# Kernel optimization log

Measured on AMD Instinct MI355X. Metric: run time of the kernel, lower is better.

The kernel has to match this reference:

```python
import jax, jax.numpy as jnp
import numpy as np


def setup_inputs() -> dict:
    key = jax.random.key(0)
    x = jax.random.normal(key, (32, 1, 1024, 1024), dtype=jnp.float32)
    return {"x": x}


def reference(x) -> jnp.ndarray:
    # Original torch loop computes a running max down the height dim (dim=2)
    # for channel 0 (C=1 here), overwriting each element with the prefix max.
    # This is exactly a cumulative-max (prefix-max scan) along axis=2.
    return jax.lax.associative_scan(jnp.maximum, x, axis=2)
```

## Files before the change

### kernel.cpp

```cpp
#include <hip/hip_runtime.h>


constexpr int B = 32;
constexpr int H = 1024;
constexpr int W = 1024;
constexpr int ROW4 = W / 4;
constexpr int SW4 = 8;
constexpr int NSTRIP = ROW4 / SW4;
constexpr int CH = 128;
constexpr int NCHUNK = H / CH;
constexpr int NT = 256;
constexpr int SEG = 32;
constexpr int RPS = CH / SEG;
constexpr int LPT = CH * SW4 / NT;

typedef float floatx4 __attribute__((ext_vector_type(4)));

__device__ __forceinline__ float4 max4(float4 a, float4 b) {
    return make_float4(fmaxf(a.x, b.x), fmaxf(a.y, b.y),
                       fmaxf(a.z, b.z), fmaxf(a.w, b.w));
}

__global__ __launch_bounds__(256) void cummax_onepass(const float* __restrict__ xf,
                                                      float* __restrict__ of) {
    __shared__ float4 buf[2][CH * SW4];
    __shared__ float4 smax[SEG][SW4];

    const int tid = threadIdx.x;
    const int b = blockIdx.x >> 5;
    const int strip = blockIdx.x & (NSTRIP - 1);
    const float4* x4 = (const float4*)xf;
    float* out_f = of;
    const size_t base4 = (size_t)b * (H * ROW4) + (size_t)strip * SW4;

    const int s = tid >> 3;
    const int wg = tid & 7;

    const float ninf = -__builtin_inff();
    float4 carry = make_float4(ninf, ninf, ninf, ninf);

    float4 ld[LPT];

#pragma unroll
    for (int i = 0; i < LPT; ++i) {
        const int e = i * NT + tid;
        const int hl = e >> 3, w = e & 7;
        ld[i] = x4[base4 + (size_t)hl * ROW4 + w];
    }
#pragma unroll
    for (int i = 0; i < LPT; ++i) buf[0][i * NT + tid] = ld[i];
    __syncthreads();

    for (int c = 0; c < NCHUNK; ++c) {
        const int cb = c & 1, nb = cb ^ 1;

        if (c + 1 < NCHUNK) {
#pragma unroll
            for (int i = 0; i < LPT; ++i) {
                const int e = i * NT + tid;
                const int hl = e >> 3, w = e & 7;
                ld[i] = x4[base4 + (size_t)((c + 1) * CH + hl) * ROW4 + w];
            }
        }

        float4 m = buf[cb][(s * RPS) * SW4 + wg];
#pragma unroll
        for (int r = 1; r < RPS; ++r) m = max4(m, buf[cb][(s * RPS + r) * SW4 + wg]);
        smax[s][wg] = m;
        __syncthreads();

        float4 pre = carry, tot = carry;
#pragma unroll
        for (int s2 = 0; s2 < SEG; ++s2) {
            const float4 v = smax[s2][wg];
            if (s2 < s) pre = max4(pre, v);
            tot = max4(tot, v);
        }
        carry = tot;

        float4 a = pre;
#pragma unroll
        for (int r = 0; r < RPS; ++r) {
            a = max4(a, buf[cb][(s * RPS + r) * SW4 + wg]);
            const size_t o = base4 + (size_t)(c * CH + s * RPS + r) * ROW4 + wg;
            floatx4 av = {a.x, a.y, a.z, a.w};
            __builtin_nontemporal_store(av, (floatx4*)out_f + o);
        }

        if (c + 1 < NCHUNK) {
#pragma unroll
            for (int i = 0; i < LPT; ++i) buf[nb][i * NT + tid] = ld[i];
        }
        __syncthreads();
    }
}

extern "C" void kernel_launch(void* const* d_in, const int* in_sizes, int n_in,
                              void* d_out, int out_size, void* d_ws, size_t ws_size,
                              hipStream_t stream) {
    const float* x = (const float*)d_in[0];
    float* out = (float*)d_out;
    cummax_onepass<<<B * NSTRIP, NT, 0, stream>>>(x, out);
}
```

Before: 257.2 us.

## Replace shared-memory chunk scan with register-resident wavefront shuffle scan

Each thread now keeps its 4 rows of the chunk in registers instead of staging the whole chunk through a double-buffered LDS tile. Segment maxima are scanned within each wavefront using shuffle-up steps, and only per-wave totals go through a small shared array. This cuts LDS traffic and removes one barrier per chunk. It also drops the nontemporal store hint, which may change cache behaviour on output writes.

```diff
diff --git a/kernel.cpp b/kernel.cpp
--- a/kernel.cpp
+++ b/kernel.cpp
@@ -9,89 +9,90 @@
 constexpr int NSTRIP = ROW4 / SW4;
 constexpr int CH = 128;
 constexpr int NCHUNK = H / CH;
-constexpr int NT = 256;
-constexpr int SEG = 32;
-constexpr int RPS = CH / SEG;
-constexpr int LPT = CH * SW4 / NT;
-
-typedef float floatx4 __attribute__((ext_vector_type(4)));
+constexpr int R = 4;
 
 __device__ __forceinline__ float4 max4(float4 a, float4 b) {
     return make_float4(fmaxf(a.x, b.x), fmaxf(a.y, b.y),
                        fmaxf(a.z, b.z), fmaxf(a.w, b.w));
 }
 
-__global__ __launch_bounds__(256) void cummax_onepass(const float* __restrict__ xf,
-                                                      float* __restrict__ of) {
-    __shared__ float4 buf[2][CH * SW4];
-    __shared__ float4 smax[SEG][SW4];
+__device__ __forceinline__ float4 shflup4(float4 v, int d) {
+    float4 r;
+    r.x = __shfl_up(v.x, d, 64);
+    r.y = __shfl_up(v.y, d, 64);
+    r.z = __shfl_up(v.z, d, 64);
+    r.w = __shfl_up(v.w, d, 64);
+    return r;
+}
+
+__global__ __launch_bounds__(256) void cummax_sp(const float* __restrict__ xf,
+                                                 float* __restrict__ of) {
+    __shared__ float4 wavetot[2][32];
 
     const int tid = threadIdx.x;
+    const int lane = tid & 63;
+    const int wid = tid >> 6;
+    const int w = tid & 7;
+    const int hsegG = tid >> 3;
+    const int hseg_l = (tid >> 3) & 7;
+
     const int b = blockIdx.x >> 5;
     const int strip = blockIdx.x & (NSTRIP - 1);
     const float4* x4 = (const float4*)xf;
-    float* out_f = of;
-    const size_t base4 = (size_t)b * (H * ROW4) + (size_t)strip * SW4;
-
-    const int s = tid >> 3;
-    const int wg = tid & 7;
+    float4* o4 = (float4*)of;
+    const size_t tbase = (size_t)b * (H * ROW4) + (size_t)strip * SW4 + w;
 
     const float ninf = -__builtin_inff();
-    float4 carry = make_float4(ninf, ninf, ninf, ninf);
+    const float4 ninf4 = make_float4(ninf, ninf, ninf, ninf);
+    float4 carry = ninf4;
 
-    float4 ld[LPT];
+    float4 cur[R], nxt[R];
 
 #pragma unroll
-    for (int i = 0; i < LPT; ++i) {
-        const int e = i * NT + tid;
-        const int hl = e >> 3, w = e & 7;
-        ld[i] = x4[base4 + (size_t)hl * ROW4 + w];
-    }
+    for (int r = 0; r < R; ++r)
+        cur[r] = x4[tbase + (size_t)(hsegG * R + r) * ROW4];
+
 #pragma unroll
-    for (int i = 0; i < LPT; ++i) buf[0][i * NT + tid] = ld[i];
-    __syncthreads();
-
     for (int c = 0; c < NCHUNK; ++c) {
-        const int cb = c & 1, nb = cb ^ 1;
-
         if (c + 1 < NCHUNK) {
 #pragma unroll
-            for (int i = 0; i < LPT; ++i) {
-                const int e = i * NT + tid;
-                const int hl = e >> 3, w = e & 7;
-                ld[i] = x4[base4 + (size_t)((c + 1) * CH + hl) * ROW4 + w];
-            }
+            for (int r = 0; r < R; ++r)
+                nxt[r] = x4[tbase + (size_t)((c + 1) * CH + hsegG * R + r) * ROW4];
         }
 
-        float4 m = buf[cb][(s * RPS) * SW4 + wg];
-#pragma unroll
-        for (int r = 1; r < RPS; ++r) m = max4(m, buf[cb][(s * RPS + r) * SW4 + wg]);
-        smax[s][wg] = m;
+        float4 m = max4(max4(cur[0], cur[1]), max4(cur[2], cur[3]));
+
+        float4 incl = m;
+        { float4 t = shflup4(incl, 8);  if (lane >= 8)  incl = max4(incl, t); }
+        { float4 t = shflup4(incl, 16); if (lane >= 16) incl = max4(incl, t); }
+        { float4 t = shflup4(incl, 32); if (lane >= 32) incl = max4(incl, t); }
+        float4 ew = shflup4(incl, 8);
+        float4 excl = (hseg_l == 0) ? ninf4 : ew;
+
+        if (hseg_l == 7) wavetot[c & 1][wid * 8 + w] = incl;
         __syncthreads();
 
-        float4 pre = carry, tot = carry;
+        float4 crosspre = carry;
+        float4 tot = carry;
 #pragma unroll
-        for (int s2 = 0; s2 < SEG; ++s2) {
-            const float4 v = smax[s2][wg];
-            if (s2 < s) pre = max4(pre, v);
+        for (int w2 = 0; w2 < 4; ++w2) {
+            float4 v = wavetot[c & 1][w2 * 8 + w];
+            if (w2 < wid) crosspre = max4(crosspre, v);
             tot = max4(tot, v);
         }
         carry = tot;
 
-        float4 a = pre;
+        float4 a = max4(crosspre, excl);
 #pragma unroll
-        for (int r = 0; r < RPS; ++r) {
-            a = max4(a, buf[cb][(s * RPS + r) * SW4 + wg]);
-            const size_t o = base4 + (size_t)(c * CH + s * RPS + r) * ROW4 + wg;
-            floatx4 av = {a.x, a.y, a.z, a.w};
-            __builtin_nontemporal_store(av, (floatx4*)out_f + o);
+        for (int r = 0; r < R; ++r) {
+            a = max4(a, cur[r]);
+            o4[tbase + (size_t)(c * CH + hsegG * R + r) * ROW4] = a;
         }
 
         if (c + 1 < NCHUNK) {
 #pragma unroll
-            for (int i = 0; i < LPT; ++i) buf[nb][i * NT + tid] = ld[i];
+            for (int r = 0; r < R; ++r) cur[r] = nxt[r];
         }
-        __syncthreads();
     }
 }
 
@@ -100,5 +101,5 @@
                               hipStream_t stream) {
     const float* x = (const float*)d_in[0];
     float* out = (float*)d_out;
-    cummax_onepass<<<B * NSTRIP, NT, 0, stream>>>(x, out);
+    cummax_sp<<<B * NSTRIP, 256, 0, stream>>>(x, out);
 }
```

Measured after the change: 240.6 us. 6.5% less time.
